# Kernel tuning notes

Hardware: AMD Instinct MI355X
Metric: run time of the kernel (lower is better)

## Reference

```python
import jax, jax.numpy as jnp
import numpy as np


def setup_inputs() -> dict:
    key = jax.random.key(0)
    k1, k2, k3, k4 = jax.random.split(key, 4)
    B, S, D_IN, D_OUT = 8, 2048, 4096, 4096
    inputs = jax.random.normal(k1, (B, S, D_IN), dtype=jnp.float32)
    # int8-valued weights stored as int32 (same math; original stores torch.int8)
    int8_weights = jax.random.randint(k2, (D_OUT, D_IN), -127, 128, dtype=jnp.int32)
    # realistic per-row dequant scales (small positive)
    scales = jax.random.uniform(k3, (D_OUT,), dtype=jnp.float32, minval=0.001, maxval=0.02)
    bias = jax.random.normal(k4, (1, D_OUT), dtype=jnp.float32) * 0.01
    return {"inputs": inputs, "int8_weights": int8_weights, "scales": scales, "bias": bias}


def reference(inputs, int8_weights, scales, bias):
    # converted_weights = int8_weights.to(inputs.dtype); F.linear(inputs, W) = inputs @ W.T
    w = int8_weights.astype(inputs.dtype)                      # [out, in]
    out = jnp.einsum('bsi,oi->bso', inputs, w)                 # [B, S, out]
    out = out * scales                                         # per-output-row scale
    out = out + bias                                           # bias broadcast [1, out]
    return out
```

## Files before the change

kernel.cpp:

```cpp
#include <hip/hip_runtime.h>
#include <hip/hip_bf16.h>

#define M_TOTAL 16384
#define N_TOTAL 4096
#define K_TOTAL 4096
#define NT (K_TOTAL / 128)

typedef __attribute__((ext_vector_type(4))) int i32x4;

__device__ __forceinline__ unsigned pack4(int a, int b, int c, int d) {
  return (a & 0xFF) | ((b & 0xFF) << 8) | ((c & 0xFF) << 16) | ((d & 0xFF) << 24);
}

__global__ __launch_bounds__(256) void quant_a(const float* __restrict__ A,
                                               unsigned* __restrict__ Aq,
                                               float* __restrict__ ascale) {
  const int row = blockIdx.x;
  const int tid = threadIdx.x;
  const float4* src = reinterpret_cast<const float4*>(A + (size_t)row * K_TOTAL);
  float4 v[4];
#pragma unroll
  for (int c = 0; c < 4; ++c) v[c] = src[tid + 256 * c];
  float amax = 0.0f;
#pragma unroll
  for (int c = 0; c < 4; ++c)
    amax = fmaxf(amax, fmaxf(fmaxf(fabsf(v[c].x), fabsf(v[c].y)),
                             fmaxf(fabsf(v[c].z), fabsf(v[c].w))));
#pragma unroll
  for (int off = 32; off > 0; off >>= 1) amax = fmaxf(amax, __shfl_xor(amax, off, 64));
  __shared__ float wmax[4];
  if ((tid & 63) == 0) wmax[tid >> 6] = amax;
  __syncthreads();
  amax = fmaxf(fmaxf(wmax[0], wmax[1]), fmaxf(wmax[2], wmax[3]));
  amax = fmaxf(amax, 1e-20f);
  const float rs = 127.0f / amax;
  if (tid == 0) ascale[row] = amax * (1.0f / 127.0f);

  unsigned* dst = Aq + (size_t)row * (K_TOTAL / 4);
#pragma unroll
  for (int c = 0; c < 4; ++c) {
    int q[4];
    float f[4] = {v[c].x, v[c].y, v[c].z, v[c].w};
#pragma unroll
    for (int i = 0; i < 4; ++i) {
      int t = (int)rintf(f[i] * rs);
      q[i] = t < -127 ? -127 : (t > 127 ? 127 : t);
    }
    dst[tid + 256 * c] = pack4(q[0], q[1], q[2], q[3]);
  }
}

__global__ void cvt_w_i8(const int* __restrict__ W, unsigned* __restrict__ Wq, int n4) {
  const int stride = gridDim.x * blockDim.x;
  for (int i = blockIdx.x * blockDim.x + threadIdx.x; i < n4; i += stride) {
    int4 v = reinterpret_cast<const int4*>(W)[i];
    Wq[i] = pack4(v.x, v.y, v.z, v.w);
  }
}

#define GLOAD_LDS16(gp, lp)                                                \
  __builtin_amdgcn_global_load_lds(                                        \
      (const __attribute__((address_space(1))) void*)(gp),                 \
      (__attribute__((address_space(3))) void*)(lp), 16, 0, 0)

#define BAR() asm volatile("s_barrier" ::: "memory")
#define VM(n) asm volatile("s_waitcnt vmcnt(" #n ")" ::: "memory")
#define SCHED0() __builtin_amdgcn_sched_barrier(0)


__global__ __launch_bounds__(512, 2) void w8a16_gemm_i8(
    const signed char* __restrict__ A,
    const signed char* __restrict__ Bt,
    const float* __restrict__ ascale,
    const float* __restrict__ scales, const float* __restrict__ bias,
    float* __restrict__ C) {
  __shared__ alignas(16) unsigned char lds[131072];

  const int tid = threadIdx.x;
  const int w = tid >> 6, l = tid & 63;
  const int wr = w >> 2, wc = w & 3;

  const int bid = blockIdx.x;
  const int swz = ((bid & 7) << 7) + (bid >> 3);
  const int bn = swz & 15, bm = swz >> 4;

  const int rowq = tid >> 3;
  const int colb = ((l & 7) ^ (l >> 3)) << 4;
  const signed char* pA = A + (size_t)(bm * 256 + rowq) * K_TOTAL + colb;
  const signed char* pB = Bt + (size_t)(bn * 256 + rowq) * K_TOTAL + colb;
  unsigned char* const ldsp = lds;
  const int woff = w << 10;

#define SDA(b_, h_) (ldsp + (b_) * 65536 + (h_) * 16384 + woff)
#define SDB(b_, h_) (ldsp + (b_) * 65536 + 32768 + (h_) * 16384 + woff)
#define STAGE_A(b_, h_, t_)                                                    \
  do {                                                                         \
    GLOAD_LDS16(pA + (size_t)((h_) * 128) * K_TOTAL + (t_) * 128, SDA(b_, h_));\
    GLOAD_LDS16(pA + (size_t)((h_) * 128 + 64) * K_TOTAL + (t_) * 128,         \
                SDA(b_, h_) + 8192);                                           \
  } while (0)
#define STAGE_B(b_, h_, t_)                                                    \
  do {                                                                         \
    GLOAD_LDS16(pB + (size_t)((h_) * 128) * K_TOTAL + (t_) * 128, SDB(b_, h_));\
    GLOAD_LDS16(pB + (size_t)((h_) * 128 + 64) * K_TOTAL + (t_) * 128,         \
                SDB(b_, h_) + 8192);                                           \
  } while (0)

  const int arow = ((l & 15) << 7) + ((((l >> 4) ^ (l & 7)) & 7) << 4);
  const int bOffC = 32768 + (wc >> 1) * 16384 + (wc & 1) * 8192;

  i32x4 af0[8], af1[8];
  i32x4 b0E[4], b0O[4], b1[4];
  i32x4 acc[8][4] = {{}};

#define RD_AF(dst_, mh_, bsel_)                                               \
  do {                                                                        \
    const unsigned char* Ab_ = ldsp + (bsel_) * 65536 + wr * 16384;           \
    _Pragma("unroll") for (int fm = 0; fm < 4; ++fm)                          \
        _Pragma("unroll") for (int kk = 0; kk < 2; ++kk)                      \
            dst_[fm * 2 + kk] = *(const i32x4*)(                              \
                Ab_ + ((mh_) * 4 + fm) * 2048 + (arow ^ (kk << 6)));          \
  } while (0)
#define RD_BH(dst_, nh_, bsel_)                                               \
  do {                                                                        \
    const unsigned char* Bb_ = ldsp + (bsel_) * 65536 + bOffC;                \
    _Pragma("unroll") for (int fn = 0; fn < 2; ++fn)                          \
        _Pragma("unroll") for (int kk = 0; kk < 2; ++kk)                      \
            dst_[fn * 2 + kk] = *(const i32x4*)(                              \
                Bb_ + ((nh_) * 2 + fn) * 2048 + (arow ^ (kk << 6)));          \
  } while (0)
#define QUAD(mh_, nh_, AF_, BF_)                                              \
  do {                                                                        \
    __builtin_amdgcn_s_setprio(1);                                            \
    _Pragma("unroll") for (int m = 0; m < 4; ++m)                             \
        _Pragma("unroll") for (int n = 0; n < 2; ++n)                         \
            _Pragma("unroll") for (int kk = 0; kk < 2; ++kk)                  \
                acc[(mh_) * 4 + m][(nh_) * 2 + n] =                           \
                    __builtin_amdgcn_mfma_i32_16x16x64_i8(                    \
                        AF_[m * 2 + kk], BF_[n * 2 + kk],                     \
                        acc[(mh_) * 4 + m][(nh_) * 2 + n], 0, 0, 0);          \
    __builtin_amdgcn_s_setprio(0);                                            \
  } while (0)

#define TILE_BODY(t_, bsel_, BNEW_, BPREV_, doprev_)                          \
  do {                                                                        \
                                                                      \
    RD_AF(af0, 0, bsel_);                                                     \
    RD_BH(BNEW_, 0, bsel_);                                                   \
    if ((t_) + 1 < NT) STAGE_A((bsel_) ^ 1, 1, (t_) + 1);                     \
    SCHED0(); BAR();                                                          \
    if (doprev_) QUAD(1, 0, af1, BPREV_);                                     \
    SCHED0(); BAR();                                                          \
                                                                      \
    RD_AF(af1, 1, bsel_);                                                     \
    RD_BH(b1, 1, bsel_);                                                      \
    SCHED0(); BAR();                                                          \
    QUAD(0, 0, af0, BNEW_);                                                   \
    SCHED0(); BAR();                                                          \
                                                                      \
    QUAD(0, 1, af0, b1);                                                      \
    SCHED0(); BAR();                                                          \
                                                                      \
    if ((t_) + 2 < NT) {                                                      \
      STAGE_B(bsel_, 0, (t_) + 2);                                            \
      STAGE_B(bsel_, 1, (t_) + 2);                                            \
      STAGE_A(bsel_, 0, (t_) + 2);                                            \
    }                                                                         \
    SCHED0(); BAR();                                                          \
    QUAD(1, 1, af1, b1);                                                      \
    if ((t_) < NT - 2) { VM(6); } else { VM(0); }                             \
    SCHED0(); BAR();                                                          \
  } while (0)

  STAGE_A(0, 0, 0); STAGE_A(0, 1, 0); STAGE_B(0, 0, 0); STAGE_B(0, 1, 0);
  STAGE_B(1, 0, 1); STAGE_B(1, 1, 1); STAGE_A(1, 0, 1);
  VM(6);
  BAR();

  for (int tt = 0; tt < NT; tt += 2) {
    TILE_BODY(tt, 0, b0E, b0O, (tt > 0));
    TILE_BODY(tt + 1, 1, b0O, b0E, 1);
  }
  QUAD(1, 0, af1, b0O);

  const int row0 = bm * 256 + wr * 128 + ((l >> 4) << 2);
  const int col0 = bn * 256 + wc * 64 + (l & 15);
#pragma unroll
  for (int fn = 0; fn < 4; ++fn) {
    const int col = col0 + fn * 16;
    const float sc = scales[col];
    const float bi = bias[col];
#pragma unroll
    for (int fm = 0; fm < 8; ++fm) {
      const int r = row0 + fm * 16;
      float* cp = C + (size_t)r * N_TOTAL + col;
#pragma unroll
      for (int j = 0; j < 4; ++j)
        cp[(size_t)j * N_TOTAL] = fmaf((float)acc[fm][fn][j], ascale[r + j] * sc, bi);
    }
  }
}

__global__ void naive_gemm(const float* __restrict__ A, const int* __restrict__ W,
                           const float* __restrict__ scales, const float* __restrict__ bias,
                           float* __restrict__ C) {
  size_t idx = (size_t)blockIdx.x * blockDim.x + threadIdx.x;
  if (idx >= (size_t)M_TOTAL * N_TOTAL) return;
  const int n = (int)(idx % N_TOTAL);
  const size_t m = idx / N_TOTAL;
  const float* a = A + m * (size_t)K_TOTAL;
  const int* w = W + (size_t)n * K_TOTAL;
  float s = 0.f;
  for (int k = 0; k < K_TOTAL; ++k) s = fmaf(a[k], (float)w[k], s);
  C[idx] = fmaf(s, scales[n], bias[n]);
}

extern "C" void kernel_launch(void* const* d_in, const int* in_sizes, int n_in,
                              void* d_out, int out_size, void* d_ws, size_t ws_size,
                              hipStream_t stream) {
  const float* A = (const float*)d_in[0];
  const int* W = (const int*)d_in[1];
  const float* scales = (const float*)d_in[2];
  const float* bias = (const float*)d_in[3];
  float* out = (float*)d_out;

  const size_t a_elems = (size_t)M_TOTAL * K_TOTAL;
  const size_t w_elems = (size_t)N_TOTAL * K_TOTAL;
  const size_t need = a_elems + w_elems + (size_t)M_TOTAL * sizeof(float);

  if (ws_size >= need) {
    signed char* A_q = (signed char*)d_ws;
    signed char* W_q = A_q + a_elems;
    float* a_s = (float*)(W_q + w_elems);
    quant_a<<<M_TOTAL, 256, 0, stream>>>(A, (unsigned*)A_q, a_s);
    cvt_w_i8<<<2048, 256, 0, stream>>>(W, (unsigned*)W_q, (int)(w_elems / 4));
    w8a16_gemm_i8<<<1024, 512, 0, stream>>>(A_q, W_q, a_s, scales, bias, out);
  } else {
    size_t total = (size_t)M_TOTAL * N_TOTAL;
    naive_gemm<<<(unsigned)((total + 255) / 256), 256, 0, stream>>>(A, W, scales, bias, out);
  }
}
```

Baseline: 414.6 us.

## Restructure int8 GEMM main loop into fewer barrier phases with prefetched fragments

Rewrites the per-tile schedule of the int8 MFMA GEMM mainloop. The first A/B fragments for the next tile are read from LDS at the end of the current tile, and the A staging for tile t+2 is split across two phases. The number of barriers and sched_group fences per tile drops from six to four, and the vmcnt wait depth is adjusted to match. This aims to overlap LDS reads and global loads with MFMAs and cut barrier stalls, at the cost of more live registers and tighter LDS-hazard reasoning.

Result: slower. 660.0 us (+59.2%).

```diff
diff --git a/kernel.cpp b/kernel.cpp
--- a/kernel.cpp
+++ b/kernel.cpp
@@ -142,46 +142,48 @@
     __builtin_amdgcn_s_setprio(0);                                            \
   } while (0)
 
-#define TILE_BODY(t_, bsel_, BNEW_, BPREV_, doprev_)                          \
-  do {                                                                        \
-                                                                      \
-    RD_AF(af0, 0, bsel_);                                                     \
-    RD_BH(BNEW_, 0, bsel_);                                                   \
-    if ((t_) + 1 < NT) STAGE_A((bsel_) ^ 1, 1, (t_) + 1);                     \
-    SCHED0(); BAR();                                                          \
-    if (doprev_) QUAD(1, 0, af1, BPREV_);                                     \
-    SCHED0(); BAR();                                                          \
+#define TILE13(t_, bsel_, B0CUR_, B0NXT_)                                     \
+  do {                                                                        \
                                                                       \
     RD_AF(af1, 1, bsel_);                                                     \
     RD_BH(b1, 1, bsel_);                                                      \
-    SCHED0(); BAR();                                                          \
-    QUAD(0, 0, af0, BNEW_);                                                   \
-    SCHED0(); BAR();                                                          \
-                                                                      \
+    SCHED0();                                                                 \
+    QUAD(0, 0, af0, B0CUR_);                                                  \
+    BAR();                                                                    \
+                                                                      \
+    if ((t_) + 2 < NT) STAGE_A(bsel_, 0, (t_) + 2);                           \
     QUAD(0, 1, af0, b1);                                                      \
-    SCHED0(); BAR();                                                          \
+    BAR();                                                                    \
                                                                       \
     if ((t_) + 2 < NT) {                                                      \
+      STAGE_A(bsel_, 1, (t_) + 2);                                            \
       STAGE_B(bsel_, 0, (t_) + 2);                                            \
       STAGE_B(bsel_, 1, (t_) + 2);                                            \
-      STAGE_A(bsel_, 0, (t_) + 2);                                            \
     }                                                                         \
-    SCHED0(); BAR();                                                          \
     QUAD(1, 1, af1, b1);                                                      \
-    if ((t_) < NT - 2) { VM(6); } else { VM(0); }                             \
-    SCHED0(); BAR();                                                          \
+    if ((t_) < NT - 2) { VM(8); } else if ((t_) == NT - 2) { VM(0); }         \
+    BAR();                                                                    \
+                                                                      \
+    if ((t_) + 1 < NT) {                                                      \
+      RD_AF(af0, 0, (bsel_) ^ 1);                                             \
+      RD_BH(B0NXT_, 0, (bsel_) ^ 1);                                          \
+    }                                                                         \
+    SCHED0();                                                                 \
+    QUAD(1, 0, af1, B0CUR_);                                                  \
+    BAR();                                                                    \
   } while (0)
 
   STAGE_A(0, 0, 0); STAGE_A(0, 1, 0); STAGE_B(0, 0, 0); STAGE_B(0, 1, 0);
-  STAGE_B(1, 0, 1); STAGE_B(1, 1, 1); STAGE_A(1, 0, 1);
-  VM(6);
+  STAGE_A(1, 0, 1); STAGE_A(1, 1, 1); STAGE_B(1, 0, 1); STAGE_B(1, 1, 1);
+  VM(8);
   BAR();
+  RD_AF(af0, 0, 0);
+  RD_BH(b0E, 0, 0);
 
   for (int tt = 0; tt < NT; tt += 2) {
-    TILE_BODY(tt, 0, b0E, b0O, (tt > 0));
-    TILE_BODY(tt + 1, 1, b0O, b0E, 1);
-  }
-  QUAD(1, 0, af1, b0O);
+    TILE13(tt, 0, b0E, b0O);
+    TILE13(tt + 1, 1, b0O, b0E);
+  }
 
   const int row0 = bm * 256 + wr * 128 + ((l >> 4) << 2);
   const int col0 = bn * 256 + wc * 64 + (l & 15);
```
